# Kernel optimization log

Hardware: AMD Instinct MI355X
Metric: run time of the kernel (lower is better)

The kernel has to match this reference:

```python
import jax, jax.numpy as jnp
import numpy as np

EPS = 1e-5

def conv2d(x, w, pad):
    # x: NCHW, w: OIHW
    return jax.lax.conv_general_dilated(
        x, w, window_strides=(1, 1), padding=[(pad, pad), (pad, pad)],
        dimension_numbers=("NCHW", "OIHW", "NCHW"))

def instnorm(x, gamma=None, beta=None):
    # per-(N,C) normalization over H,W (biased variance, like torch InstanceNorm2d)
    mu = jnp.mean(x, axis=(2, 3), keepdims=True)
    var = jnp.mean((x - mu) ** 2, axis=(2, 3), keepdims=True)
    y = (x - mu) * jax.lax.rsqrt(var + EPS)
    if gamma is not None:
        y = y * gamma[None, :, None, None] + beta[None, :, None, None]
    return y

def ode_rhs(y, W, b):
    # conv -> relu -> instance norm (no affine) -> conv_transpose(same weight) -> -1 (stable)
    z = conv2d(y, W, 1) + b[None, :, None, None]
    z = jax.nn.relu(z)
    z = instnorm(z)
    # ConvTranspose2d with weight W (in,out,kh,kw here square C,C) == conv with
    # channel-swapped, spatially flipped kernel, SAME padding.
    Wt = jnp.transpose(jnp.flip(W, axis=(2, 3)), (1, 0, 2, 3))
    z = conv2d(z, Wt, 1)
    return -z

def ode_block(y, Wbank, bbank):
    # RK4 over t_grid = linspace(0,1,5): 4 steps of dt = 0.25.
    # Piecewise-constant weights: floor(t*4) clamped -> stages 1-3 of step i use
    # bank[i]; stage 4 (at t_{i+1}) uses bank[min(i+1, 3)].
    n = Wbank.shape[0]
    dt = 1.0 / n
    for i in range(n):
        j = min(i + 1, n - 1)
        k1 = ode_rhs(y, Wbank[i], bbank[i])
        k2 = ode_rhs(y + 0.5 * dt * k1, Wbank[i], bbank[i])
        k3 = ode_rhs(y + 0.5 * dt * k2, Wbank[i], bbank[i])
        k4 = ode_rhs(y + dt * k3, Wbank[j], bbank[j])
        y = y + (dt / 6.0) * (k1 + 2.0 * k2 + 2.0 * k3 + k4)
    return y

def avgpool2(x):
    N, C, H, W = x.shape
    return x.reshape(N, C, H // 2, 2, W // 2, 2).mean(axis=(3, 5))

def forward(x, stem_w, stem_b, norm1_g, norm1_b, ode1_W, ode1_b,
            conn1_w, conn1_b, norm3_g, norm3_b, ode2_W, ode2_b,
            conn2_w, conn2_b, norm4_g, norm4_b, ode3_W, ode3_b,
            head_w, head_b):
    x = conv2d(x, stem_w, 1) + stem_b[None, :, None, None]
    x = instnorm(x, norm1_g, norm1_b)
    x = jax.nn.relu(x)
    x = ode_block(x, ode1_W, ode1_b)
    x = conv2d(x, conn1_w, 0) + conn1_b[None, :, None, None]
    x = instnorm(x, norm3_g, norm3_b)
    x = jax.nn.relu(x)
    x = avgpool2(x)
    x = ode_block(x, ode2_W, ode2_b)
    x = conv2d(x, conn2_w, 0) + conn2_b[None, :, None, None]
    x = instnorm(x, norm4_g, norm4_b)
    x = jax.nn.relu(x)
    x = avgpool2(x)
    x = ode_block(x, ode3_W, ode3_b)
    x = x.mean(axis=(2, 3))  # AdaptiveAvgPool2d(1) + Flatten -> [N, 4*ch]
    return x @ head_w.T + head_b

def setup_inputs() -> dict:
    key = jax.random.key(0)
    ks = jax.random.split(key, 16)
    ch = 64
    f = jnp.float32
    d = {
        "x": jax.random.normal(ks[0], (8, 3, 96, 96), f),
        "stem_w": jax.random.normal(ks[1], (ch, 3, 3, 3), f) * 0.1,
        "stem_b": jnp.zeros((ch,), f),
        "norm1_g": jnp.ones((ch,), f),
        "norm1_b": jnp.zeros((ch,), f),
        "ode1_W": jax.random.normal(ks[2], (4, ch, ch, 3, 3), f) * 0.1,
        "ode1_b": jnp.zeros((4, ch), f),
        "conn1_w": jax.random.normal(ks[3], (2 * ch, ch, 1, 1), f) * 0.1,
        "conn1_b": jnp.zeros((2 * ch,), f),
        "norm3_g": jnp.ones((2 * ch,), f),
        "norm3_b": jnp.zeros((2 * ch,), f),
        "ode2_W": jax.random.normal(ks[4], (4, 2 * ch, 2 * ch, 3, 3), f) * 0.1,
        "ode2_b": jnp.zeros((4, 2 * ch), f),
        "conn2_w": jax.random.normal(ks[5], (4 * ch, 2 * ch, 1, 1), f) * 0.1,
        "conn2_b": jnp.zeros((4 * ch,), f),
        "norm4_g": jnp.ones((4 * ch,), f),
        "norm4_b": jnp.zeros((4 * ch,), f),
        "ode3_W": jax.random.normal(ks[6], (4, 4 * ch, 4 * ch, 3, 3), f) * 0.1,
        "ode3_b": jnp.zeros((4, 4 * ch), f),
        "head_w": jax.random.normal(ks[7], (10, 4 * ch), f) * 0.05,
        "head_b": jnp.zeros((10,), f),
    }
    return d

def reference(x, stem_w, stem_b, norm1_g, norm1_b, ode1_W, ode1_b,
              conn1_w, conn1_b, norm3_g, norm3_b, ode2_W, ode2_b,
              conn2_w, conn2_b, norm4_g, norm4_b, ode3_W, ode3_b,
              head_w, head_b):
    return forward(x, stem_w, stem_b, norm1_g, norm1_b, ode1_W, ode1_b,
                   conn1_w, conn1_b, norm3_g, norm3_b, ode2_W, ode2_b,
                   conn2_w, conn2_b, norm4_g, norm4_b, ode3_W, ode3_b,
                   head_w, head_b)
```

## Files before the change

### kernel.cpp

```cpp
#include <hip/hip_runtime.h>


typedef __attribute__((ext_vector_type(8)))  short  s16x8;
typedef __attribute__((ext_vector_type(16))) float  f32x16;

__device__ __forceinline__ unsigned short bf16_rtne(float f) {
    unsigned u = __builtin_bit_cast(unsigned, f);
    unsigned r = u + 0x7FFFu + ((u >> 16) & 1u);
    return (unsigned short)(r >> 16);
}
__device__ __forceinline__ void split2(float v, unsigned& h, unsigned& l) {
    unsigned u = __builtin_bit_cast(unsigned, v);
    h = (u + 0x7fffu + ((u >> 16) & 1u)) >> 16;
    float r = v - __builtin_bit_cast(float, h << 16);
    unsigned ur = __builtin_bit_cast(unsigned, r);
    l = (ur + 0x7fffu + ((ur >> 16) & 1u)) >> 16;
}
__device__ __forceinline__ unsigned packsplit(float v) {
    unsigned h, l; split2(v, h, l); return h | (l << 16);
}

__global__ __launch_bounds__(256) void pack_weights(
    const float* __restrict__ Wb, unsigned short* __restrict__ out, int C)
{
    const int dir = blockIdx.y;
    const int MT = C >> 5, ICC = C >> 4;
    const size_t TOT = (size_t)36 * C * C;
    size_t t = (size_t)blockIdx.x * 256 + threadIdx.x;
    if (t >= TOT) return;
    int j = t & 7;
    int l = (t >> 3) & 63;
    size_t r = t >> 9;
    int kp  = r % 9;  r /= 9;
    int mt  = r % MT; r /= MT;
    int icc = r % ICC; r /= ICC;
    int bank = (int)r;
    int oc = mt * 32 + (l & 31);
    int ic = icc * 16 + (l >> 5) * 8 + j;
    int kh = kp / 3, kw = kp % 3;
    float v;
    if (dir == 0)
        v = Wb[(((size_t)(bank * C + oc) * C + ic) * 3 + kh) * 3 + kw];
    else
        v = Wb[(((size_t)(bank * C + ic) * C + oc) * 3 + (2 - kh)) * 3 + (2 - kw)];
    unsigned short h = bf16_rtne(v);
    float hf = __builtin_bit_cast(float, (unsigned)h << 16);
    unsigned short lo = bf16_rtne(v - hf);
    size_t idx = ((((size_t)bank * ICC + icc) * MT + mt) * 9 + kp) * 1024 + l * 8 + j;
    unsigned short* base = out + (size_t)dir * 72 * C * C;
    base[idx] = h;
    base[idx + 512] = lo;
}

template<int NW, int MODE>
__global__ __launch_bounds__(NW * 64) void conv_mfma4(
    const void* __restrict__ in,
    const unsigned short* __restrict__ pA,
    const float* __restrict__ bias,
    const float* __restrict__ sums_in,
    float* __restrict__ sums_out,
    const float* __restrict__ ybase, float* __restrict__ accb,
    float* __restrict__ ydstF, unsigned* __restrict__ ydstS,
    int C, int H, int W, int tilesX, int NCtot, float inv_hw,
    int mode, float acoef, float dt6)
{
    constexpr bool CONV2 = (MODE == 2);
    constexpr int TPX = 16, TPY = 2 * NW;
    constexpr int HX = TPX + 2, HY = TPY + 2;
    constexpr int NROW = HX * HY;
    constexpr int RS = 20;
    constexpr int PL = NROW * RS;
    constexpr int BUFS = 2 * PL;
    constexpr int NTHR = NW * 64;
    constexpr int NELEM = NROW * 16;
    constexpr int NIT = (NELEM + NTHR - 1) / NTHR;
    __shared__ __align__(16) unsigned short sB[2 * BUFS];
    __shared__ float sTab[CONV2 ? 512 : 4];

    const int tid = threadIdx.x;
    const int w = tid >> 6, lane = tid & 63;
    const int n = blockIdx.x;
    const int tile = blockIdx.y;
    const int mt = blockIdx.z;
    const int tileX = tile % tilesX, tileY = tile / tilesX;
    const int px0 = tileX * TPX, py0 = tileY * TPY;
    const int ocb = mt * 32;
    const int HW = H * W;
    const int ICC = C >> 4, MT = C >> 5;
    const int col = lane & 31, half = lane >> 5;
    const int xl = col & 15, yr = col >> 4;
    const int wy0 = 2 * w;
    const int ncbase = n * C;

    float stg[NIT];
    auto stageLoad = [&](int icc) {
#pragma unroll
        for (int i = 0; i < NIT; i++) {
            int e = tid + i * NTHR;
            float v = 0.f;
            if (e < NELEM) {
                int ic = e / NROW; int r = e - ic * NROW;
                int yy = r / HX, xx = r - yy * HX;
                int gy = py0 + yy - 1, gx = px0 + xx - 1;
                if (gy >= 0 && gy < H && gx >= 0 && gx < W) {
                    int c = icc * 16 + ic;
                    size_t ad = (size_t)(ncbase + c) * HW + gy * W + gx;
                    if (MODE == 0)
                        v = ((const float*)in)[ad];
                    else
                        v = __builtin_bit_cast(float, ((const unsigned*)in)[ad]);
                }
            }
            stg[i] = v;
        }
    };
    auto stageWrite = [&](int b, int c0) {
#pragma unroll
        for (int i = 0; i < NIT; i++) {
            int e = tid + i * NTHR;
            if (e < NELEM) {
                int ic = e / NROW; int r = e - ic * NROW;
                unsigned h, l;
                if (MODE == 1) {
                    unsigned u = __builtin_bit_cast(unsigned, stg[i]);
                    h = u & 0xffffu; l = u >> 16;
                } else if (MODE == 2) {
                    int yy = r / HX, xx = r - yy * HX;
                    int gy = py0 + yy - 1, gx = px0 + xx - 1;
                    float v = 0.f;
                    if (gy >= 0 && gy < H && gx >= 0 && gx < W) {
                        unsigned u = __builtin_bit_cast(unsigned, stg[i]);
                        float vh = __builtin_bit_cast(float, u << 16);
                        float vl = __builtin_bit_cast(float, u & 0xffff0000u);
                        int c = c0 + ic;
                        v = (vh + vl - sTab[2 * c]) * sTab[2 * c + 1];
                    }
                    split2(v, h, l);
                } else {
                    split2(stg[i], h, l);
                }
                int off = b * BUFS + r * RS + ic;
                sB[off] = (unsigned short)h;
                sB[off + PL] = (unsigned short)l;
            }
        }
    };
    auto loadB = [&](int b, int kp, s16x8& oh, s16x8& ol) {
        int kh = kp / 3, kw = kp - kh * 3;
        int px = (wy0 + yr + kh) * HX + (xl + kw);
        int off = b * BUFS + px * RS + half * 8;
        oh = *(const s16x8*)&sB[off];
        ol = *(const s16x8*)&sB[off + PL];
    };

    f32x16 accA{}, accB{}, accC{};

    stageLoad(0);

    if (CONV2 && blockIdx.x == 0 && blockIdx.y == 0) {
        int per = (2 * NCtot + MT - 1) / MT;
        int st = mt * per;
        int en = st + per; if (en > 2 * NCtot) en = 2 * NCtot;
        for (int i = st + tid; i < en; i += NTHR) sums_out[i] = 0.f;
    }
    if (CONV2) {
        for (int c0 = tid; c0 < C; c0 += NTHR) {
            float s = sums_in[ncbase + c0];
            float q = sums_in[NCtot + ncbase + c0];
            float m = s * inv_hw;
            sTab[2 * c0] = m;
            sTab[2 * c0 + 1] = rsqrtf(fmaf(-m, m, q * inv_hw) + 1e-5f);
        }
        __syncthreads();
    }

    stageWrite(0, 0);
    __syncthreads();

    for (int icc = 0; icc < ICC; ++icc) {
        s16x8 aH[9], aL[9];
        {
            const unsigned short* ab =
                pA + ((size_t)(icc * MT + mt)) * 9216 + lane * 8;
#pragma unroll
            for (int kp = 0; kp < 9; ++kp) {
                aH[kp] = *(const s16x8*)(ab + kp * 1024);
                aL[kp] = *(const s16x8*)(ab + kp * 1024 + 512);
            }
        }
        const int b = icc & 1;
        if (icc + 1 < ICC) stageLoad(icc + 1);

        s16x8 bh, bl;
        loadB(b, 0, bh, bl);
#pragma unroll
        for (int kp = 0; kp < 9; ++kp) {
            s16x8 bhn, bln;
            if (kp < 8) loadB(b, kp + 1, bhn, bln);
            accA = __builtin_amdgcn_mfma_f32_32x32x16_bf16(aH[kp], bh, accA, 0, 0, 0);
            accB = __builtin_amdgcn_mfma_f32_32x32x16_bf16(aL[kp], bh, accB, 0, 0, 0);
            accC = __builtin_amdgcn_mfma_f32_32x32x16_bf16(aH[kp], bl, accC, 0, 0, 0);
            if (kp < 8) { bh = bhn; bl = bln; }
        }
        if (icc + 1 < ICC) {
            stageWrite(b ^ 1, (icc + 1) * 16);
            __syncthreads();
        }
    }

    const int gx = px0 + xl;
    const int gy = py0 + wy0 + yr;
    const bool valid = (gx < W);
    float* sred = (float*)sB;
#pragma unroll
    for (int r = 0; r < 16; r++) {
        int row = (r & 3) + 8 * (r >> 2) + 4 * half;
        int oc = ocb + row;
        size_t idx = (size_t)(ncbase + oc) * HW + (size_t)gy * W + gx;
        float v = accA[r] + accB[r] + accC[r];
        if (!CONV2) {
            v += bias[oc];
            v = fmaxf(v, 0.f);
            if (valid) ydstS[idx] = packsplit(v);
            float s = valid ? v : 0.f;
            float sq = s * s;
#pragma unroll
            for (int m = 1; m < 32; m <<= 1) {
                s  += __shfl_xor(s, m, 64);
                sq += __shfl_xor(sq, m, 64);
            }
            if ((lane & 31) == 0) {
                int slot = ((w * 2 + half) * 16 + r) * 2;
                sred[slot] = s;
                sred[slot + 1] = sq;
            }
        } else if (valid) {
            float k = -v;
            if (mode == 0) {
                accb[idx] = k;
                ydstS[idx] = packsplit(ybase[idx] + acoef * k);
            } else if (mode == 3) {
                ydstF[idx] = ybase[idx] + dt6 * (accb[idx] + k);
            } else {
                accb[idx] += 2.f * k;
                ydstS[idx] = packsplit(ybase[idx] + acoef * k);
            }
        }
    }
    if (!CONV2) {
        __syncthreads();
        if (tid < 32) {
            int h2 = (tid >> 2) & 1;
            int r  = (tid & 3) | ((tid >> 3) << 2);
            float s = 0.f, sq = 0.f;
#pragma unroll
            for (int wv = 0; wv < NW; wv++) {
                int slot = ((wv * 2 + h2) * 16 + r) * 2;
                s  += sred[slot];
                sq += sred[slot + 1];
            }
            atomicAdd(&sums_out[ncbase + ocb + tid], s);
            atomicAdd(&sums_out[NCtot + ncbase + ocb + tid], sq);
        }
    }
}

#define TS  16
#define OCT 16
#define CIT 8
__global__ __launch_bounds__(256) void conv3x3_kernel(
    const float* __restrict__ in, const float* __restrict__ w,
    const float* __restrict__ bias, float* __restrict__ out,
    int N, int Cin, int Cout, int H, int W, int tilesX, int relu)
{
    __shared__ float sIn[CIT][TS + 2][TS + 2];
    __shared__ float sW[OCT][CIT][9];
    const int tid = threadIdx.x;
    const int tx = tid & (TS - 1), ty = tid >> 4;
    const int tileX = blockIdx.x % tilesX, tileY = blockIdx.x / tilesX;
    const int x0 = tileX * TS, y0 = tileY * TS;
    const int oc0 = blockIdx.y * OCT;
    const int n = blockIdx.z;
    const int HW = H * W;

    float acc[OCT];
#pragma unroll
    for (int o = 0; o < OCT; o++) acc[o] = 0.f;

    for (int ic0 = 0; ic0 < Cin; ic0 += CIT) {
        for (int idx = tid; idx < CIT * (TS + 2) * (TS + 2); idx += 256) {
            int c  = idx / ((TS + 2) * (TS + 2));
            int r  = idx % ((TS + 2) * (TS + 2));
            int iy = r / (TS + 2), ix = r % (TS + 2);
            int gy = y0 + iy - 1, gx = x0 + ix - 1;
            int ic = ic0 + c;
            float v = 0.f;
            if (ic < Cin && gy >= 0 && gy < H && gx >= 0 && gx < W)
                v = in[(size_t)(n * Cin + ic) * HW + gy * W + gx];
            sIn[c][iy][ix] = v;
        }
        for (int idx = tid; idx < OCT * CIT * 9; idx += 256) {
            int o = idx / (CIT * 9);
            int r = idx % (CIT * 9);
            int c = r / 9, k = r % 9;
            int oc = oc0 + o, ic = ic0 + c;
            sW[o][c][k] = (oc < Cout && ic < Cin)
                              ? w[((size_t)oc * Cin + ic) * 9 + k] : 0.f;
        }
        __syncthreads();
#pragma unroll
        for (int c = 0; c < CIT; c++)
#pragma unroll
            for (int kh = 0; kh < 3; kh++)
#pragma unroll
                for (int kw = 0; kw < 3; kw++) {
                    float v = sIn[c][ty + kh][tx + kw];
#pragma unroll
                    for (int o = 0; o < OCT; o++)
                        acc[o] = fmaf(v, sW[o][c][kh * 3 + kw], acc[o]);
                }
        __syncthreads();
    }

    int gy = y0 + ty, gx = x0 + tx;
    if (gy < H && gx < W) {
#pragma unroll
        for (int o = 0; o < OCT; o++) {
            int oc = oc0 + o;
            if (oc < Cout) {
                float v = acc[o] + bias[oc];
                if (relu) v = fmaxf(v, 0.f);
                out[(size_t)(n * Cout + oc) * HW + gy * W + gx] = v;
            }
        }
    }
}

__global__ __launch_bounds__(256) void stats_kernel(
    const float* __restrict__ x, float* __restrict__ mu, float* __restrict__ rstd,
    int HW, float inv_hw)
{
    int nc = blockIdx.x;
    const float* p = x + (size_t)nc * HW;
    float s = 0.f, ss = 0.f;
    for (int i = threadIdx.x; i < HW; i += 256) {
        float v = p[i];
        s += v;
        ss = fmaf(v, v, ss);
    }
    for (int off = 32; off; off >>= 1) {
        s  += __shfl_down(s, off, 64);
        ss += __shfl_down(ss, off, 64);
    }
    __shared__ float aS[4], aSS[4];
    int wid = threadIdx.x >> 6, lane = threadIdx.x & 63;
    if (lane == 0) { aS[wid] = s; aSS[wid] = ss; }
    __syncthreads();
    if (threadIdx.x == 0) {
        s  = aS[0] + aS[1] + aS[2] + aS[3];
        ss = aSS[0] + aSS[1] + aSS[2] + aSS[3];
        float m = s * inv_hw;
        float var = fmaf(-m, m, ss * inv_hw);
        mu[nc] = m;
        rstd[nc] = rsqrtf(var + 1e-5f);
    }
}

__global__ __launch_bounds__(256) void norm_affine_relu_kernel(
    const float* __restrict__ in, float* __restrict__ out,
    const float* __restrict__ mu, const float* __restrict__ rstd,
    const float* __restrict__ g, const float* __restrict__ b,
    int C, int HW, size_t total)
{
    size_t i = (size_t)blockIdx.x * 256 + threadIdx.x;
    if (i >= total) return;
    size_t nc = i / HW;
    int c = (int)(nc % C);
    float v = (in[i] - mu[nc]) * rstd[nc] * g[c] + b[c];
    out[i] = fmaxf(v, 0.f);
}

__global__ __launch_bounds__(256) void avgpool2_kernel(
    const float* __restrict__ in, float* __restrict__ out,
    int Ho, int Wo, size_t total)
{
    size_t i = (size_t)blockIdx.x * 256 + threadIdx.x;
    if (i >= total) return;
    int wo = (int)(i % Wo);
    int ho = (int)((i / Wo) % Ho);
    size_t nc = i / ((size_t)Wo * Ho);
    const float* p = in + nc * (size_t)(4 * Ho * Wo) + (size_t)(2 * ho) * (2 * Wo) + 2 * wo;
    out[i] = 0.25f * (p[0] + p[1] + p[2 * Wo] + p[2 * Wo + 1]);
}

#define C1OCT 8
__global__ __launch_bounds__(256) void conv1x1_kernel(
    const float* __restrict__ in, const float* __restrict__ w,
    const float* __restrict__ bias, float* __restrict__ out,
    int Cin, int Cout, int HW)
{
    int p = blockIdx.x * 256 + threadIdx.x;
    int oc0 = blockIdx.y * C1OCT;
    int n = blockIdx.z;
    if (p >= HW) return;
    float acc[C1OCT];
#pragma unroll
    for (int o = 0; o < C1OCT; o++) acc[o] = 0.f;
    const float* ip = in + (size_t)n * Cin * HW + p;
    for (int ic = 0; ic < Cin; ic++) {
        float v = ip[(size_t)ic * HW];
#pragma unroll
        for (int o = 0; o < C1OCT; o++)
            acc[o] = fmaf(v, w[(size_t)(oc0 + o) * Cin + ic], acc[o]);
    }
    float* op = out + ((size_t)n * Cout + oc0) * HW + p;
#pragma unroll
    for (int o = 0; o < C1OCT; o++) op[(size_t)o * HW] = acc[o] + bias[oc0 + o];
}

__global__ __launch_bounds__(128) void head_kernel(
    const float* __restrict__ m, const float* __restrict__ hw,
    const float* __restrict__ hb, float* __restrict__ out, int C)
{
    int t = threadIdx.x;
    if (t < 80) {
        int n = t / 10, k = t % 10;
        float acc = hb[k];
        for (int c = 0; c < C; c++)
            acc = fmaf(m[n * C + c], hw[k * C + c], acc);
        out[t] = acc;
    }
}

struct OdeCfg { int C, H, tilesX, tilesT; };
static const OdeCfg CFG[3] = {
    {64, 96, 6, 36},
    {128, 48, 3, 18},
    {256, 24, 2, 6},
};

static void launch_c1(int st, int inMode, const void* in, const unsigned short* pA,
                      const float* bias, float* sums_w, unsigned* z, hipStream_t s)
{
    const OdeCfg& c = CFG[st];
    dim3 g(8, c.tilesT, c.C / 32);
    float ih = 1.f / (c.H * c.H);
    if (st == 0) {
        if (inMode == 0)
            conv_mfma4<8, 0><<<g, 512, 0, s>>>(in, pA, bias,
                nullptr, sums_w, nullptr, nullptr, nullptr, z,
                c.C, c.H, c.H, c.tilesX, 8 * c.C, ih, 0, 0.f, 0.f);
        else
            conv_mfma4<8, 1><<<g, 512, 0, s>>>(in, pA, bias,
                nullptr, sums_w, nullptr, nullptr, nullptr, z,
                c.C, c.H, c.H, c.tilesX, 8 * c.C, ih, 0, 0.f, 0.f);
    } else {
        if (inMode == 0)
            conv_mfma4<4, 0><<<g, 256, 0, s>>>(in, pA, bias,
                nullptr, sums_w, nullptr, nullptr, nullptr, z,
                c.C, c.H, c.H, c.tilesX, 8 * c.C, ih, 0, 0.f, 0.f);
        else
            conv_mfma4<4, 1><<<g, 256, 0, s>>>(in, pA, bias,
                nullptr, sums_w, nullptr, nullptr, nullptr, z,
                c.C, c.H, c.H, c.tilesX, 8 * c.C, ih, 0, 0.f, 0.f);
    }
}

static void launch_c2(int st, const unsigned* z, const unsigned short* pA,
                      const float* sums_r, float* sums_z,
                      const float* ybase, float* accb,
                      float* ydstF, unsigned* ydstS,
                      int mode, float acoef, hipStream_t s)
{
    const OdeCfg& c = CFG[st];
    dim3 g(8, c.tilesT, c.C / 32);
    float ih = 1.f / (c.H * c.H);
    const float dt6 = 0.25f / 6.f;
    if (st == 0)
        conv_mfma4<8, 2><<<g, 512, 0, s>>>(z, pA, nullptr,
            sums_r, sums_z, ybase, accb, ydstF, ydstS,
            c.C, c.H, c.H, c.tilesX, 8 * c.C, ih, mode, acoef, dt6);
    else
        conv_mfma4<4, 2><<<g, 256, 0, s>>>(z, pA, nullptr,
            sums_r, sums_z, ybase, accb, ydstF, ydstS,
            c.C, c.H, c.H, c.tilesX, 8 * c.C, ih, mode, acoef, dt6);
}

static void ode_block_mfma(int st, float* y, unsigned* t, unsigned* z, float* a,
                           float* sums, int& par, unsigned short* pack,
                           const float* bbank, hipStream_t s)
{
    const OdeCfg& c = CFG[st];
    const int C = c.C;
    const size_t BANKW = (size_t)18 * C * C;
    const size_t DIRW  = (size_t)72 * C * C;
    const float dt = 0.25f;
    for (int i = 0; i < 4; i++) {
        int j = (i + 1 > 3) ? 3 : i + 1;
        const unsigned short* p1  = pack + i * BANKW;
        const unsigned short* p1t = pack + DIRW + i * BANKW;
        const unsigned short* p4  = pack + j * BANKW;
        const unsigned short* p4t = pack + DIRW + j * BANKW;
        const float* b1 = bbank + (size_t)i * C;
        const float* b4 = bbank + (size_t)j * C;

        launch_c1(st, 0, y, p1, b1, sums + par * 4096, z, s);
        launch_c2(st, z, p1t, sums + par * 4096, sums + (par ^ 1) * 4096,
                  y, a, nullptr, t, 0, 0.5f * dt, s);
        par ^= 1;
        launch_c1(st, 1, t, p1, b1, sums + par * 4096, z, s);
        launch_c2(st, z, p1t, sums + par * 4096, sums + (par ^ 1) * 4096,
                  y, a, nullptr, t, 1, 0.5f * dt, s);
        par ^= 1;
        launch_c1(st, 1, t, p1, b1, sums + par * 4096, z, s);
        launch_c2(st, z, p1t, sums + par * 4096, sums + (par ^ 1) * 4096,
                  y, a, nullptr, t, 1, dt, s);
        par ^= 1;
        launch_c1(st, 1, t, p4, b4, sums + par * 4096, z, s);
        launch_c2(st, z, p4t, sums + par * 4096, sums + (par ^ 1) * 4096,
                  y, a, y, t, 3, 0.f, s);
        par ^= 1;
    }
}

extern "C" void kernel_launch(void* const* d_in, const int* in_sizes, int n_in,
                              void* d_out, int out_size, void* d_ws, size_t ws_size,
                              hipStream_t stream)
{
    const float* x       = (const float*)d_in[0];
    const float* stem_w  = (const float*)d_in[1];
    const float* stem_b  = (const float*)d_in[2];
    const float* norm1_g = (const float*)d_in[3];
    const float* norm1_b = (const float*)d_in[4];
    const float* ode1_W  = (const float*)d_in[5];
    const float* ode1_b  = (const float*)d_in[6];
    const float* conn1_w = (const float*)d_in[7];
    const float* conn1_b = (const float*)d_in[8];
    const float* norm3_g = (const float*)d_in[9];
    const float* norm3_b = (const float*)d_in[10];
    const float* ode2_W  = (const float*)d_in[11];
    const float* ode2_b  = (const float*)d_in[12];
    const float* conn2_w = (const float*)d_in[13];
    const float* conn2_b = (const float*)d_in[14];
    const float* norm4_g = (const float*)d_in[15];
    const float* norm4_b = (const float*)d_in[16];
    const float* ode3_W  = (const float*)d_in[17];
    const float* ode3_b  = (const float*)d_in[18];
    const float* head_w  = (const float*)d_in[19];
    const float* head_b  = (const float*)d_in[20];
    float* out = (float*)d_out;

    float* ws = (float*)d_ws;
    const size_t BUF = 4718592;
    float*    y  = ws;
    unsigned* t  = (unsigned*)(ws + BUF);
    unsigned* z  = (unsigned*)(ws + 2 * BUF);
    float*    a  = ws + 3 * BUF;
    float*    mu = ws + 4 * BUF;
    float*    rs = mu + 2048;
    float*    sums = ws + 4 * BUF + 4096;
    unsigned short* pack = (unsigned short*)(ws + 4 * BUF + 4096 + 8192);
    float* tf = (float*)t;

    hipMemsetAsync(sums, 0, 8192 * sizeof(float), stream);
    int par = 0;

    {
        int H = 96, tiles = 6;
        dim3 grid(tiles * tiles, 64 / OCT, 8);
        conv3x3_kernel<<<grid, 256, 0, stream>>>(x, stem_w, stem_b, (float*)z,
                                                 8, 3, 64, H, H, tiles, 0);
        stats_kernel<<<8 * 64, 256, 0, stream>>>((float*)z, mu, rs, H * H, 1.f / (H * H));
        size_t total = (size_t)8 * 64 * H * H;
        norm_affine_relu_kernel<<<(total + 255) / 256, 256, 0, stream>>>(
            (float*)z, y, mu, rs, norm1_g, norm1_b, 64, H * H, total);
    }

    {
        size_t TOT = (size_t)36 * 64 * 64;
        pack_weights<<<dim3((TOT + 255) / 256, 2), 256, 0, stream>>>(ode1_W, pack, 64);
        ode_block_mfma(0, y, t, z, a, sums, par, pack, ode1_b, stream);
    }

    {
        int H = 96, HW = H * H, Cin = 64, Cout = 128;
        dim3 grid((HW + 255) / 256, Cout / C1OCT, 8);
        conv1x1_kernel<<<grid, 256, 0, stream>>>(y, conn1_w, conn1_b, tf, Cin, Cout, HW);
        stats_kernel<<<8 * Cout, 256, 0, stream>>>(tf, mu, rs, HW, 1.f / HW);
        size_t total = (size_t)8 * Cout * HW;
        norm_affine_relu_kernel<<<(total + 255) / 256, 256, 0, stream>>>(
            tf, tf, mu, rs, norm3_g, norm3_b, Cout, HW, total);
        size_t ptotal = (size_t)8 * Cout * 48 * 48;
        avgpool2_kernel<<<(ptotal + 255) / 256, 256, 0, stream>>>(tf, y, 48, 48, ptotal);
    }

    {
        size_t TOT = (size_t)36 * 128 * 128;
        pack_weights<<<dim3((TOT + 255) / 256, 2), 256, 0, stream>>>(ode2_W, pack, 128);
        ode_block_mfma(1, y, t, z, a, sums, par, pack, ode2_b, stream);
    }

    {
        int H = 48, HW = H * H, Cin = 128, Cout = 256;
        dim3 grid((HW + 255) / 256, Cout / C1OCT, 8);
        conv1x1_kernel<<<grid, 256, 0, stream>>>(y, conn2_w, conn2_b, tf, Cin, Cout, HW);
        stats_kernel<<<8 * Cout, 256, 0, stream>>>(tf, mu, rs, HW, 1.f / HW);
        size_t total = (size_t)8 * Cout * HW;
        norm_affine_relu_kernel<<<(total + 255) / 256, 256, 0, stream>>>(
            tf, tf, mu, rs, norm4_g, norm4_b, Cout, HW, total);
        size_t ptotal = (size_t)8 * Cout * 24 * 24;
        avgpool2_kernel<<<(ptotal + 255) / 256, 256, 0, stream>>>(tf, y, 24, 24, ptotal);
    }

    {
        size_t TOT = (size_t)36 * 256 * 256;
        pack_weights<<<dim3((TOT + 255) / 256, 2), 256, 0, stream>>>(ode3_W, pack, 256);
        ode_block_mfma(2, y, t, z, a, sums, par, pack, ode3_b, stream);
    }

    {
        int H = 24, HW = H * H, C = 256;
        stats_kernel<<<8 * C, 256, 0, stream>>>(y, mu, rs, HW, 1.f / HW);
        head_kernel<<<1, 128, 0, stream>>>(mu, head_w, head_b, out, C);
    }
}
```

Measured before the change: 5.374 ms.

## Replace atomic stats with per-tile partials, fuse norm+pool, vectorize stem and 1x1

Instance-norm statistics in the ODE convs are now written as per-tile partial sums and reduced by the consuming conv, replacing atomics, ping-pong buffers and the memset. The normalize-affine-relu pass is fused into the avgpool after each connector. The stem conv gets a dedicated kernel computing two pixels per thread, and the 1x1 conv uses float4 loads and stores. These cut atomic contention and memory passes, but each consumer now runs a serial loop over tiles to finish the reduction.

```diff
diff --git a/kernel.cpp b/kernel.cpp
--- a/kernel.cpp
+++ b/kernel.cpp
@@ -57,11 +57,11 @@
     const void* __restrict__ in,
     const unsigned short* __restrict__ pA,
     const float* __restrict__ bias,
-    const float* __restrict__ sums_in,
-    float* __restrict__ sums_out,
+    const float* __restrict__ partI,
+    float* __restrict__ partO,
     const float* __restrict__ ybase, float* __restrict__ accb,
     float* __restrict__ ydstF, unsigned* __restrict__ ydstS,
-    int C, int H, int W, int tilesX, int NCtot, float inv_hw,
+    int C, int H, int W, int tilesX, int tilesT, float inv_hw,
     int mode, float acoef, float dt6)
 {
     constexpr bool CONV2 = (MODE == 2);
@@ -157,16 +157,16 @@
 
     stageLoad(0);
 
-    if (CONV2 && blockIdx.x == 0 && blockIdx.y == 0) {
-        int per = (2 * NCtot + MT - 1) / MT;
-        int st = mt * per;
-        int en = st + per; if (en > 2 * NCtot) en = 2 * NCtot;
-        for (int i = st + tid; i < en; i += NTHR) sums_out[i] = 0.f;
-    }
     if (CONV2) {
         for (int c0 = tid; c0 < C; c0 += NTHR) {
-            float s = sums_in[ncbase + c0];
-            float q = sums_in[NCtot + ncbase + c0];
+            int mtc = c0 >> 5, occ = c0 & 31;
+            const float* pb = partI + ((size_t)(n * MT + mtc) * tilesT) * 64 + occ;
+            float s = 0.f, q = 0.f;
+#pragma unroll 4
+            for (int tt = 0; tt < tilesT; ++tt) {
+                s += pb[(size_t)tt * 64];
+                q += pb[(size_t)tt * 64 + 32];
+            }
             float m = s * inv_hw;
             sTab[2 * c0] = m;
             sTab[2 * c0 + 1] = rsqrtf(fmaf(-m, m, q * inv_hw) + 1e-5f);
@@ -259,80 +259,69 @@
                 s  += sred[slot];
                 sq += sred[slot + 1];
             }
-            atomicAdd(&sums_out[ncbase + ocb + tid], s);
-            atomicAdd(&sums_out[NCtot + ncbase + ocb + tid], sq);
-        }
-    }
-}
-
-#define TS  16
-#define OCT 16
-#define CIT 8
-__global__ __launch_bounds__(256) void conv3x3_kernel(
+            float* po = partO + ((size_t)(n * MT + mt) * tilesT + tile) * 64;
+            po[tid] = s;
+            po[tid + 32] = sq;
+        }
+    }
+}
+
+__global__ __launch_bounds__(256) void conv3x3_stem(
     const float* __restrict__ in, const float* __restrict__ w,
     const float* __restrict__ bias, float* __restrict__ out,
-    int N, int Cin, int Cout, int H, int W, int tilesX, int relu)
-{
-    __shared__ float sIn[CIT][TS + 2][TS + 2];
-    __shared__ float sW[OCT][CIT][9];
+    int H, int W, int tilesX)
+{
+    __shared__ float sIn[3][18][34];
+    __shared__ float sW[16][3][9];
     const int tid = threadIdx.x;
-    const int tx = tid & (TS - 1), ty = tid >> 4;
+    const int tx = tid & 15, ty = tid >> 4;
     const int tileX = blockIdx.x % tilesX, tileY = blockIdx.x / tilesX;
-    const int x0 = tileX * TS, y0 = tileY * TS;
-    const int oc0 = blockIdx.y * OCT;
+    const int x0 = tileX * 32, y0 = tileY * 16;
+    const int oc0 = blockIdx.y * 16;
     const int n = blockIdx.z;
     const int HW = H * W;
 
-    float acc[OCT];
-#pragma unroll
-    for (int o = 0; o < OCT; o++) acc[o] = 0.f;
-
-    for (int ic0 = 0; ic0 < Cin; ic0 += CIT) {
-        for (int idx = tid; idx < CIT * (TS + 2) * (TS + 2); idx += 256) {
-            int c  = idx / ((TS + 2) * (TS + 2));
-            int r  = idx % ((TS + 2) * (TS + 2));
-            int iy = r / (TS + 2), ix = r % (TS + 2);
-            int gy = y0 + iy - 1, gx = x0 + ix - 1;
-            int ic = ic0 + c;
-            float v = 0.f;
-            if (ic < Cin && gy >= 0 && gy < H && gx >= 0 && gx < W)
-                v = in[(size_t)(n * Cin + ic) * HW + gy * W + gx];
-            sIn[c][iy][ix] = v;
-        }
-        for (int idx = tid; idx < OCT * CIT * 9; idx += 256) {
-            int o = idx / (CIT * 9);
-            int r = idx % (CIT * 9);
-            int c = r / 9, k = r % 9;
-            int oc = oc0 + o, ic = ic0 + c;
-            sW[o][c][k] = (oc < Cout && ic < Cin)
-                              ? w[((size_t)oc * Cin + ic) * 9 + k] : 0.f;
-        }
-        __syncthreads();
-#pragma unroll
-        for (int c = 0; c < CIT; c++)
-#pragma unroll
-            for (int kh = 0; kh < 3; kh++)
-#pragma unroll
-                for (int kw = 0; kw < 3; kw++) {
-                    float v = sIn[c][ty + kh][tx + kw];
-#pragma unroll
-                    for (int o = 0; o < OCT; o++)
-                        acc[o] = fmaf(v, sW[o][c][kh * 3 + kw], acc[o]);
+    for (int idx = tid; idx < 3 * 18 * 34; idx += 256) {
+        int c = idx / (18 * 34); int r = idx % (18 * 34);
+        int iy = r / 34, ix = r % 34;
+        int gy = y0 + iy - 1, gx = x0 + ix - 1;
+        float v = 0.f;
+        if (gy >= 0 && gy < H && gx >= 0 && gx < W)
+            v = in[(size_t)(n * 3 + c) * HW + gy * W + gx];
+        sIn[c][iy][ix] = v;
+    }
+    for (int idx = tid; idx < 16 * 27; idx += 256) {
+        int o = idx / 27, r = idx % 27;
+        sW[o][r / 9][r % 9] = w[(size_t)(oc0 + o) * 27 + r];
+    }
+    __syncthreads();
+
+    float a0[16], a1[16];
+#pragma unroll
+    for (int o = 0; o < 16; o++) { a0[o] = 0.f; a1[o] = 0.f; }
+#pragma unroll
+    for (int c = 0; c < 3; c++)
+#pragma unroll
+        for (int kh = 0; kh < 3; kh++)
+#pragma unroll
+            for (int kw = 0; kw < 3; kw++) {
+                float v0 = sIn[c][ty + kh][tx + kw];
+                float v1 = sIn[c][ty + kh][tx + 16 + kw];
+#pragma unroll
+                for (int o = 0; o < 16; o++) {
+                    float wv = sW[o][c][kh * 3 + kw];
+                    a0[o] = fmaf(v0, wv, a0[o]);
+                    a1[o] = fmaf(v1, wv, a1[o]);
                 }
-        __syncthreads();
-    }
-
-    int gy = y0 + ty, gx = x0 + tx;
-    if (gy < H && gx < W) {
-#pragma unroll
-        for (int o = 0; o < OCT; o++) {
-            int oc = oc0 + o;
-            if (oc < Cout) {
-                float v = acc[o] + bias[oc];
-                if (relu) v = fmaxf(v, 0.f);
-                out[(size_t)(n * Cout + oc) * HW + gy * W + gx] = v;
-            }
-        }
+            }
+
+    const int gy = y0 + ty, gx = x0 + tx;
+#pragma unroll
+    for (int o = 0; o < 16; o++) {
+        float bb = bias[oc0 + o];
+        size_t base = (size_t)(n * 64 + oc0 + o) * HW + (size_t)gy * W + gx;
+        out[base] = a0[o] + bb;
+        out[base + 16] = a1[o] + bb;
     }
 }
 
@@ -380,17 +369,27 @@
     out[i] = fmaxf(v, 0.f);
 }
 
-__global__ __launch_bounds__(256) void avgpool2_kernel(
+__global__ __launch_bounds__(256) void norm_pool_kernel(
     const float* __restrict__ in, float* __restrict__ out,
-    int Ho, int Wo, size_t total)
+    const float* __restrict__ mu, const float* __restrict__ rstd,
+    const float* __restrict__ g, const float* __restrict__ b,
+    int C, int Ho, int Wo, size_t total)
 {
     size_t i = (size_t)blockIdx.x * 256 + threadIdx.x;
     if (i >= total) return;
     int wo = (int)(i % Wo);
     int ho = (int)((i / Wo) % Ho);
     size_t nc = i / ((size_t)Wo * Ho);
-    const float* p = in + nc * (size_t)(4 * Ho * Wo) + (size_t)(2 * ho) * (2 * Wo) + 2 * wo;
-    out[i] = 0.25f * (p[0] + p[1] + p[2 * Wo] + p[2 * Wo + 1]);
+    int c = (int)(nc % C);
+    const int Wi = 2 * Wo;
+    const float* p = in + nc * (size_t)(4 * Ho * Wo) + (size_t)(2 * ho) * Wi + 2 * wo;
+    float sc  = rstd[nc] * g[c];
+    float off = fmaf(-mu[nc], sc, b[c]);
+    float2 t0 = *(const float2*)p;
+    float2 t1 = *(const float2*)(p + Wi);
+    float s = fmaxf(fmaf(t0.x, sc, off), 0.f) + fmaxf(fmaf(t0.y, sc, off), 0.f)
+            + fmaxf(fmaf(t1.x, sc, off), 0.f) + fmaxf(fmaf(t1.y, sc, off), 0.f);
+    out[i] = 0.25f * s;
 }
 
 #define C1OCT 8
@@ -399,23 +398,37 @@
     const float* __restrict__ bias, float* __restrict__ out,
     int Cin, int Cout, int HW)
 {
+    const int HW4 = HW >> 2;
     int p = blockIdx.x * 256 + threadIdx.x;
-    int oc0 = blockIdx.y * C1OCT;
-    int n = blockIdx.z;
-    if (p >= HW) return;
-    float acc[C1OCT];
-#pragma unroll
-    for (int o = 0; o < C1OCT; o++) acc[o] = 0.f;
-    const float* ip = in + (size_t)n * Cin * HW + p;
+    if (p >= HW4) return;
+    const int oc0 = blockIdx.y * C1OCT;
+    const int n = blockIdx.z;
+    const float4* ip = (const float4*)(in + (size_t)n * Cin * HW) + p;
+    float acc[C1OCT][4];
+#pragma unroll
+    for (int o = 0; o < C1OCT; o++)
+        acc[o][0] = acc[o][1] = acc[o][2] = acc[o][3] = 0.f;
+#pragma unroll 4
     for (int ic = 0; ic < Cin; ic++) {
-        float v = ip[(size_t)ic * HW];
-#pragma unroll
-        for (int o = 0; o < C1OCT; o++)
-            acc[o] = fmaf(v, w[(size_t)(oc0 + o) * Cin + ic], acc[o]);
-    }
-    float* op = out + ((size_t)n * Cout + oc0) * HW + p;
-#pragma unroll
-    for (int o = 0; o < C1OCT; o++) op[(size_t)o * HW] = acc[o] + bias[oc0 + o];
+        float4 v = ip[(size_t)ic * HW4];
+#pragma unroll
+        for (int o = 0; o < C1OCT; o++) {
+            float wv = w[(size_t)(oc0 + o) * Cin + ic];
+            acc[o][0] = fmaf(v.x, wv, acc[o][0]);
+            acc[o][1] = fmaf(v.y, wv, acc[o][1]);
+            acc[o][2] = fmaf(v.z, wv, acc[o][2]);
+            acc[o][3] = fmaf(v.w, wv, acc[o][3]);
+        }
+    }
+    float4* op = (float4*)(out + ((size_t)n * Cout + oc0) * HW) + p;
+#pragma unroll
+    for (int o = 0; o < C1OCT; o++) {
+        float bb = bias[oc0 + o];
+        float4 r;
+        r.x = acc[o][0] + bb; r.y = acc[o][1] + bb;
+        r.z = acc[o][2] + bb; r.w = acc[o][3] + bb;
+        op[(size_t)o * HW4] = r;
+    }
 }
 
 __global__ __launch_bounds__(128) void head_kernel(
@@ -440,7 +453,7 @@
 };
 
 static void launch_c1(int st, int inMode, const void* in, const unsigned short* pA,
-                      const float* bias, float* sums_w, unsigned* z, hipStream_t s)
+                      const float* bias, float* part, unsigned* z, hipStream_t s)
 {
     const OdeCfg& c = CFG[st];
     dim3 g(8, c.tilesT, c.C / 32);
@@ -448,26 +461,26 @@
     if (st == 0) {
         if (inMode == 0)
             conv_mfma4<8, 0><<<g, 512, 0, s>>>(in, pA, bias,
-                nullptr, sums_w, nullptr, nullptr, nullptr, z,
-                c.C, c.H, c.H, c.tilesX, 8 * c.C, ih, 0, 0.f, 0.f);
+                nullptr, part, nullptr, nullptr, nullptr, z,
+                c.C, c.H, c.H, c.tilesX, c.tilesT, ih, 0, 0.f, 0.f);
         else
             conv_mfma4<8, 1><<<g, 512, 0, s>>>(in, pA, bias,
-                nullptr, sums_w, nullptr, nullptr, nullptr, z,
-                c.C, c.H, c.H, c.tilesX, 8 * c.C, ih, 0, 0.f, 0.f);
+                nullptr, part, nullptr, nullptr, nullptr, z,
+                c.C, c.H, c.H, c.tilesX, c.tilesT, ih, 0, 0.f, 0.f);
     } else {
         if (inMode == 0)
             conv_mfma4<4, 0><<<g, 256, 0, s>>>(in, pA, bias,
-                nullptr, sums_w, nullptr, nullptr, nullptr, z,
-                c.C, c.H, c.H, c.tilesX, 8 * c.C, ih, 0, 0.f, 0.f);
+                nullptr, part, nullptr, nullptr, nullptr, z,
+                c.C, c.H, c.H, c.tilesX, c.tilesT, ih, 0, 0.f, 0.f);
         else
             conv_mfma4<4, 1><<<g, 256, 0, s>>>(in, pA, bias,
-                nullptr, sums_w, nullptr, nullptr, nullptr, z,
-                c.C, c.H, c.H, c.tilesX, 8 * c.C, ih, 0, 0.f, 0.f);
+                nullptr, part, nullptr, nullptr, nullptr, z,
+                c.C, c.H, c.H, c.tilesX, c.tilesT, ih, 0, 0.f, 0.f);
     }
 }
 
 static void launch_c2(int st, const unsigned* z, const unsigned short* pA,
-                      const float* sums_r, float* sums_z,
+                      const float* part,
                       const float* ybase, float* accb,
                       float* ydstF, unsigned* ydstS,
                       int mode, float acoef, hipStream_t s)
@@ -478,16 +491,16 @@
     const float dt6 = 0.25f / 6.f;
     if (st == 0)
         conv_mfma4<8, 2><<<g, 512, 0, s>>>(z, pA, nullptr,
-            sums_r, sums_z, ybase, accb, ydstF, ydstS,
-            c.C, c.H, c.H, c.tilesX, 8 * c.C, ih, mode, acoef, dt6);
+            part, nullptr, ybase, accb, ydstF, ydstS,
+            c.C, c.H, c.H, c.tilesX, c.tilesT, ih, mode, acoef, dt6);
     else
         conv_mfma4<4, 2><<<g, 256, 0, s>>>(z, pA, nullptr,
-            sums_r, sums_z, ybase, accb, ydstF, ydstS,
-            c.C, c.H, c.H, c.tilesX, 8 * c.C, ih, mode, acoef, dt6);
+            part, nullptr, ybase, accb, ydstF, ydstS,
+            c.C, c.H, c.H, c.tilesX, c.tilesT, ih, mode, acoef, dt6);
 }
 
 static void ode_block_mfma(int st, float* y, unsigned* t, unsigned* z, float* a,
-                           float* sums, int& par, unsigned short* pack,
+                           float* part, unsigned short* pack,
                            const float* bbank, hipStream_t s)
 {
     const OdeCfg& c = CFG[st];
@@ -504,22 +517,14 @@
         const float* b1 = bbank + (size_t)i * C;
         const float* b4 = bbank + (size_t)j * C;
 
-        launch_c1(st, 0, y, p1, b1, sums + par * 4096, z, s);
-        launch_c2(st, z, p1t, sums + par * 4096, sums + (par ^ 1) * 4096,
-                  y, a, nullptr, t, 0, 0.5f * dt, s);
-        par ^= 1;
-        launch_c1(st, 1, t, p1, b1, sums + par * 4096, z, s);
-        launch_c2(st, z, p1t, sums + par * 4096, sums + (par ^ 1) * 4096,
-                  y, a, nullptr, t, 1, 0.5f * dt, s);
-        par ^= 1;
-        launch_c1(st, 1, t, p1, b1, sums + par * 4096, z, s);
-        launch_c2(st, z, p1t, sums + par * 4096, sums + (par ^ 1) * 4096,
-                  y, a, nullptr, t, 1, dt, s);
-        par ^= 1;
-        launch_c1(st, 1, t, p4, b4, sums + par * 4096, z, s);
-        launch_c2(st, z, p4t, sums + par * 4096, sums + (par ^ 1) * 4096,
-                  y, a, y, t, 3, 0.f, s);
-        par ^= 1;
+        launch_c1(st, 0, y, p1, b1, part, z, s);
+        launch_c2(st, z, p1t, part, y, a, nullptr, t, 0, 0.5f * dt, s);
+        launch_c1(st, 1, t, p1, b1, part, z, s);
+        launch_c2(st, z, p1t, part, y, a, nullptr, t, 1, 0.5f * dt, s);
+        launch_c1(st, 1, t, p1, b1, part, z, s);
+        launch_c2(st, z, p1t, part, y, a, nullptr, t, 1, dt, s);
+        launch_c1(st, 1, t, p4, b4, part, z, s);
+        launch_c2(st, z, p4t, part, y, a, y, t, 3, 0.f, s);
     }
 }
 
@@ -558,18 +563,15 @@
     float*    a  = ws + 3 * BUF;
     float*    mu = ws + 4 * BUF;
     float*    rs = mu + 2048;
-    float*    sums = ws + 4 * BUF + 4096;
-    unsigned short* pack = (unsigned short*)(ws + 4 * BUF + 4096 + 8192);
+    float*    part = ws + 4 * BUF + 4096;
+    unsigned short* pack = (unsigned short*)(ws + 4 * BUF + 4096 + 36864);
     float* tf = (float*)t;
 
-    hipMemsetAsync(sums, 0, 8192 * sizeof(float), stream);
-    int par = 0;
-
     {
-        int H = 96, tiles = 6;
-        dim3 grid(tiles * tiles, 64 / OCT, 8);
-        conv3x3_kernel<<<grid, 256, 0, stream>>>(x, stem_w, stem_b, (float*)z,
-                                                 8, 3, 64, H, H, tiles, 0);
+        int H = 96;
+        dim3 grid(3 * 6, 4, 8);
+        conv3x3_stem<<<grid, 256, 0, stream>>>(x, stem_w, stem_b, (float*)z,
+                                               H, H, 3);
         stats_kernel<<<8 * 64, 256, 0, stream>>>((float*)z, mu, rs, H * H, 1.f / (H * H));
         size_t total = (size_t)8 * 64 * H * H;
         norm_affine_relu_kernel<<<(total + 255) / 256, 256, 0, stream>>>(
@@ -579,43 +581,39 @@
     {
         size_t TOT = (size_t)36 * 64 * 64;
         pack_weights<<<dim3((TOT + 255) / 256, 2), 256, 0, stream>>>(ode1_W, pack, 64);
-        ode_block_mfma(0, y, t, z, a, sums, par, pack, ode1_b, stream);
+        ode_block_mfma(0, y, t, z, a, part, pack, ode1_b, stream);
     }
 
     {
         int H = 96, HW = H * H, Cin = 64, Cout = 128;
-        dim3 grid((HW + 255) / 256, Cout / C1OCT, 8);
+        dim3 grid((HW / 4 + 255) / 256, Cout / C1OCT, 8);
         conv1x1_kernel<<<grid, 256, 0, stream>>>(y, conn1_w, conn1_b, tf, Cin, Cout, HW);
         stats_kernel<<<8 * Cout, 256, 0, stream>>>(tf, mu, rs, HW, 1.f / HW);
-        size_t total = (size_t)8 * Cout * HW;
-        norm_affine_relu_kernel<<<(total + 255) / 256, 256, 0, stream>>>(
-            tf, tf, mu, rs, norm3_g, norm3_b, Cout, HW, total);
         size_t ptotal = (size_t)8 * Cout * 48 * 48;
-        avgpool2_kernel<<<(ptotal + 255) / 256, 256, 0, stream>>>(tf, y, 48, 48, ptotal);
+        norm_pool_kernel<<<(ptotal + 255) / 256, 256, 0, stream>>>(
+            tf, y, mu, rs, norm3_g, norm3_b, Cout, 48, 48, ptotal);
     }
 
     {
         size_t TOT = (size_t)36 * 128 * 128;
         pack_weights<<<dim3((TOT + 255) / 256, 2), 256, 0, stream>>>(ode2_W, pack, 128);
-        ode_block_mfma(1, y, t, z, a, sums, par, pack, ode2_b, stream);
+        ode_block_mfma(1, y, t, z, a, part, pack, ode2_b, stream);
     }
 
     {
         int H = 48, HW = H * H, Cin = 128, Cout = 256;
-        dim3 grid((HW + 255) / 256, Cout / C1OCT, 8);
+        dim3 grid((HW / 4 + 255) / 256, Cout / C1OCT, 8);
         conv1x1_kernel<<<grid, 256, 0, stream>>>(y, conn2_w, conn2_b, tf, Cin, Cout, HW);
         stats_kernel<<<8 * Cout, 256, 0, stream>>>(tf, mu, rs, HW, 1.f / HW);
-        size_t total = (size_t)8 * Cout * HW;
-        norm_affine_relu_kernel<<<(total + 255) / 256, 256, 0, stream>>>(
-            tf, tf, mu, rs, norm4_g, norm4_b, Cout, HW, total);
         size_t ptotal = (size_t)8 * Cout * 24 * 24;
-        avgpool2_kernel<<<(ptotal + 255) / 256, 256, 0, stream>>>(tf, y, 24, 24, ptotal);
+        norm_pool_kernel<<<(ptotal + 255) / 256, 256, 0, stream>>>(
+            tf, y, mu, rs, norm4_g, norm4_b, Cout, 24, 24, ptotal);
     }
 
     {
         size_t TOT = (size_t)36 * 256 * 256;
         pack_weights<<<dim3((TOT + 255) / 256, 2), 256, 0, stream>>>(ode3_W, pack, 256);
-        ode_block_mfma(2, y, t, z, a, sums, par, pack, ode3_b, stream);
+        ode_block_mfma(2, y, t, z, a, part, pack, ode3_b, stream);
     }
 
     {
```

New measurement: 5.394 ms. No clear change (+0.4%).
